# Kernel tuning notes

Measured on AMD Instinct MI355X. Metric: run time of the kernel, lower is better.

Reference implementation:

```python
import jax, jax.numpy as jnp
import numpy as np

N_EMBD = 768
HEAD_SIZE = 64

def setup_inputs() -> dict:
    key = jax.random.key(0)
    k1, k2, k3, k4 = jax.random.split(key, 4)
    B, T = 8, 2048
    x = jax.random.normal(k1, (B, T, N_EMBD), dtype=jnp.float32)
    s = 1.0 / np.sqrt(N_EMBD)
    Wk = jax.random.normal(k2, (N_EMBD, HEAD_SIZE), dtype=jnp.float32) * s
    Wq = jax.random.normal(k3, (N_EMBD, HEAD_SIZE), dtype=jnp.float32) * s
    Wv = jax.random.normal(k4, (N_EMBD, HEAD_SIZE), dtype=jnp.float32) * s
    return {"x": x, "Wk": Wk, "Wq": Wq, "Wv": Wv}

def reference(x, Wk, Wq, Wv):
    # x: [B, T, C]; projections: [B, T, H]
    B, T, C = x.shape
    k = jnp.einsum('btc,ch->bth', x, Wk)
    q = jnp.einsum('btc,ch->bth', x, Wq)
    v = jnp.einsum('btc,ch->bth', x, Wv)
    # scores [B, T, T], scaled by head_size^-0.5
    wei = jnp.einsum('bth,bsh->bts', q, k) * (HEAD_SIZE ** -0.5)
    causal = jnp.tril(jnp.ones((T, T), dtype=bool))
    wei = jnp.where(causal, wei, -jnp.inf)
    wei = jax.nn.softmax(wei, axis=-1)
    # dropout omitted (eval mode / deterministic reference)
    out = jnp.einsum('bts,bsh->bth', wei, v)
    return out
```

## Files before the change

### kernel.cpp

```cpp
#include <hip/hip_runtime.h>

#define B_ 8
#define T_ 2048
#define C_ 768
#define H_ 64
#define QT_ (T_ / 64)
#define NCH_ 8

typedef __bf16 bf16x8 __attribute__((ext_vector_type(8)));
typedef unsigned short ushort8 __attribute__((ext_vector_type(8)));
typedef float f32x4 __attribute__((ext_vector_type(4)));
typedef float f32x16 __attribute__((ext_vector_type(16)));

typedef __attribute__((address_space(1))) const void g_void;
typedef __attribute__((address_space(3))) void lds_void;

static __device__ __forceinline__ unsigned short f32_to_bf16(float f) {
  unsigned int u = __float_as_uint(f);
  u += 0x7FFFu + ((u >> 16) & 1u);
  return (unsigned short)(u >> 16);
}

static __device__ __forceinline__ float bf16_to_f32(unsigned short u) {
  return __uint_as_float(((unsigned int)u) << 16);
}

static __device__ __forceinline__ unsigned int cvtpk_bf16(float a, float b) {
  unsigned int r;
  asm("v_cvt_pk_bf16_f32 %0, %1, %2" : "=v"(r) : "v"(a), "v"(b));
  return r;
}

static __device__ __forceinline__ f32x4 mfma16(ushort8 a, ushort8 b, f32x4 c) {
  return __builtin_amdgcn_mfma_f32_16x16x32_bf16(
      __builtin_bit_cast(bf16x8, a), __builtin_bit_cast(bf16x8, b), c, 0, 0, 0);
}

static __device__ __forceinline__ f32x16 mfma32(ushort8 a, ushort8 b, f32x16 c) {
  return __builtin_amdgcn_mfma_f32_32x32x16_bf16(
      __builtin_bit_cast(bf16x8, a), __builtin_bit_cast(bf16x8, b), c, 0, 0, 0);
}

template <int BASE>
static __device__ __forceinline__ ushort8 packA(const f32x16& p) {
  unsigned int a1 = cvtpk_bf16(p[BASE + 0], p[BASE + 1]);
  unsigned int a2 = cvtpk_bf16(p[BASE + 2], p[BASE + 3]);
  unsigned int a3 = cvtpk_bf16(p[BASE + 4], p[BASE + 5]);
  unsigned int a4 = cvtpk_bf16(p[BASE + 6], p[BASE + 7]);
  asm("v_permlane32_swap_b32 %0, %1" : "+v"(a1), "+v"(a3));
  asm("v_permlane32_swap_b32 %0, %1" : "+v"(a2), "+v"(a4));
  uint4 w = {a1, a2, a3, a4};
  return __builtin_bit_cast(ushort8, w);
}

__global__ void prep_w_kernel(const float* __restrict__ Wk, const float* __restrict__ Wq,
                              const float* __restrict__ Wv, unsigned short* __restrict__ Wt) {
  int g = blockIdx.x * 256 + threadIdx.x;
  if (g >= 24 * 768) return;
  int ks = g / 768, s = g - ks * 768;
  int n = s >> 2, perm = s & 3;
  int k8 = perm ^ (n & 3) ^ ((n >> 2) & 3);
  int p = n >> 6, col = n & 63;
  const float* W = (p == 0) ? Wk : (p == 1) ? Wq : Wv;
  float sc = (p == 1) ? 0.125f * 1.44269504088896f : 1.0f;
  int kbase = ks * 32 + k8 * 8;
  ushort8 v;
#pragma unroll
  for (int e = 0; e < 8; ++e) v[e] = f32_to_bf16(W[(kbase + e) * 64 + col] * sc);
  *(ushort8*)(Wt + (size_t)g * 8) = v;
}

__global__ __launch_bounds__(512) void proj_kernel(
    const float* __restrict__ x, const unsigned short* __restrict__ Wt,
    unsigned short* __restrict__ Qb, unsigned short* __restrict__ Kb,
    unsigned short* __restrict__ Vt) {
  __shared__ unsigned short Wl[2][6144];
  __shared__ unsigned short Xl[2][1024];
  const int tid = threadIdx.x;
  const int wave = tid >> 6, lane = tid & 63;
  const int lo = lane & 15, hi = lane >> 4;
  const int rg = wave & 1, ch3 = wave >> 1;
  const int row0 = blockIdx.x * 32;

  f32x4 acc[3];
#pragma unroll
  for (int t = 0; t < 3; ++t) acc[t] = (f32x4){0.f, 0.f, 0.f, 0.f};

  const int xr = (tid & 127) >> 2;
  const int xk8 = tid & 3;
  const int xslot = xr * 4 + (xk8 ^ (xr & 3) ^ ((xr >> 2) & 3));
  const float* xsrc = x + (size_t)(row0 + xr) * C_ + xk8 * 8;

  const int arow = rg * 16 + lo;
  const int aaddr = (arow * 4 + (hi ^ (arow & 3) ^ ((arow >> 2) & 3))) * 8;

  auto wstage = [&](int buf, int ks) {
    const unsigned short* base = Wt + (size_t)ks * 6144 + lane * 8;
    for (int is = wave; is < 12; is += 8)
      __builtin_amdgcn_global_load_lds((g_void*)(base + is * 512),
          (lds_void*)(&Wl[buf][is * 512]), 16, 0, 0);
  };

  float4 xa0 = {}, xa1 = {}, xb0 = {}, xb1 = {};

  wstage(0, 0);
  if (tid < 128) {
    xa0 = *(const float4*)(xsrc);
    xa1 = *(const float4*)(xsrc + 4);
  }

  for (int ks = 0; ks < 24; ++ks) {
    const int cur = ks & 1;
    asm volatile("s_waitcnt vmcnt(0)" ::: "memory");
    __syncthreads();
    if (ks + 1 < 24) {
      wstage(cur ^ 1, ks + 1);
      if (tid < 128) {
        xb0 = *(const float4*)(xsrc + (ks + 1) * 32);
        xb1 = *(const float4*)(xsrc + (ks + 1) * 32 + 4);
      }
    }
    if (tid < 128) {
      unsigned int dd[4];
      dd[0] = cvtpk_bf16(xa0.x, xa0.y);
      dd[1] = cvtpk_bf16(xa0.z, xa0.w);
      dd[2] = cvtpk_bf16(xa1.x, xa1.y);
      dd[3] = cvtpk_bf16(xa1.z, xa1.w);
      *(uint4*)(&Xl[cur][xslot * 8]) = *(uint4*)dd;
    }
    __syncthreads();
    ushort8 af = *(const ushort8*)(&Xl[cur][aaddr]);
#pragma unroll
    for (int t = 0; t < 3; ++t) {
      const int n = ch3 * 48 + t * 16 + lo;
      const int baddr = (n * 4 + (hi ^ (n & 3) ^ ((n >> 2) & 3))) * 8;
      ushort8 bfr = *(const ushort8*)(&Wl[cur][baddr]);
      acc[t] = mfma16(af, bfr, acc[t]);
    }
    xa0 = xb0; xa1 = xb1;
  }

#pragma unroll
  for (int t = 0; t < 3; ++t) {
    const int n = ch3 * 48 + t * 16 + lo;
    const int p = n >> 6, nn = n & 63;
#pragma unroll
    for (int r = 0; r < 4; ++r) {
      const int rgl = row0 + rg * 16 + hi * 4 + r;
      unsigned short val = f32_to_bf16(acc[t][r]);
      if (p == 0) {
        Kb[rgl * H_ + nn] = val;
      } else if (p == 1) {
        Qb[rgl * H_ + nn] = val;
      } else {
        const int b = rgl >> 11;
        const int tt = rgl & (T_ - 1);
        Vt[((b * H_ + nn) << 11) + tt] = val;
      }
    }
  }
}

__global__ __launch_bounds__(128) void attn_part_kernel(
    const unsigned short* __restrict__ Qb, const unsigned short* __restrict__ Kb,
    const unsigned short* __restrict__ Vt, unsigned short* __restrict__ Opb,
    float* __restrict__ Ml) {
  const int qt = blockIdx.x;
  const int b = blockIdx.y;
  const int ch = blockIdx.z;
  const int t0 = ch * 4;
  if (t0 > qt) return;
  const int t1 = min(qt, t0 + 3);

  __shared__ __align__(16) unsigned short Kl[2][4096];
  __shared__ __align__(16) unsigned short Vl[2][4096];

  const int tid = threadIdx.x;
  const int wave = tid >> 6;
  const int lane = tid & 63;
  const int il = lane & 31;
  const int h = lane >> 5;
  const int i0w = qt * 64 + wave * 32;
  const size_t bt = (size_t)b * T_;

  const int srow = tid >> 3;
  const int sslot = (tid & 7) ^ (srow & 7);

  ushort8 qf[4];
#pragma unroll
  for (int dc = 0; dc < 4; ++dc)
    qf[dc] = *(const ushort8*)(Qb + (bt + i0w + il) * 64 + dc * 16 + h * 8);

  f32x16 o0 = {}, o1 = {};
  float m = -1e30f, lsum = 0.f;

  auto stage = [&](int buf, int jt) {
    const int j0 = jt * 64;
#pragma unroll
    for (int is = 0; is < 4; ++is) {
      const unsigned short* gK = Kb + ((bt + j0 + is * 16 + srow) << 6) + (sslot << 3);
      __builtin_amdgcn_global_load_lds((g_void*)gK,
          (lds_void*)(&Kl[buf][is * 1024 + wave * 512]), 16, 0, 0);
    }
#pragma unroll
    for (int is = 0; is < 4; ++is) {
      const unsigned short* gV = Vt + (((size_t)(b * H_ + is * 16 + srow)) << 11) + j0 + (sslot << 3);
      __builtin_amdgcn_global_load_lds((g_void*)gV,
          (lds_void*)(&Vl[buf][is * 1024 + wave * 512]), 16, 0, 0);
    }
  };

  stage(0, t0);

  for (int jt = t0; jt <= t1; ++jt) {
    const int cur = (jt - t0) & 1;
    asm volatile("s_waitcnt vmcnt(0)" ::: "memory");
    __syncthreads();
    if (jt < t1) stage(cur ^ 1, jt + 1);
    const int j0 = jt * 64;

    f32x16 s0 = {}, s1 = {};
    __builtin_amdgcn_s_setprio(1);
#pragma unroll
    for (int dc = 0; dc < 4; ++dc) {
      const int swz = ((dc * 2 + h) ^ (il & 7)) << 3;
      ushort8 k0 = *(const ushort8*)(&Kl[cur][(il << 6) + swz]);
      ushort8 k1 = *(const ushort8*)(&Kl[cur][((32 + il) << 6) + swz]);
      s0 = mfma32(k0, qf[dc], s0);
      s1 = mfma32(k1, qf[dc], s1);
    }
    __builtin_amdgcn_s_setprio(0);

    if (jt == qt) {
      const int ig = i0w + il;
#pragma unroll
      for (int r = 0; r < 16; ++r) {
        const int jl = j0 + (r & 3) + 8 * (r >> 2) + 4 * h;
        if (jl > ig) s0[r] = -1e30f;
        if (jl + 32 > ig) s1[r] = -1e30f;
      }
    }

    float mx[8];
#pragma unroll
    for (int r = 0; r < 8; ++r) mx[r] = fmaxf(fmaxf(s0[r], s0[r + 8]), fmaxf(s1[r], s1[r + 8]));
#pragma unroll
    for (int d = 4; d >= 1; d >>= 1)
#pragma unroll
      for (int r = 0; r < d; ++r) mx[r] = fmaxf(mx[r], mx[r + d]);
    float tm = fmaxf(mx[0], __shfl_xor(mx[0], 32));
    const float mnew = fmaxf(m, tm);
    const float scl = exp2f(m - mnew);
    m = mnew;
    float sa = 0.f, sb = 0.f, sc2 = 0.f, sd = 0.f;
#pragma unroll
    for (int r = 0; r < 16; r += 4) {
      s0[r] = exp2f(s0[r] - mnew);     sa += s0[r];
      s0[r + 1] = exp2f(s0[r + 1] - mnew); sb += s0[r + 1];
      s0[r + 2] = exp2f(s0[r + 2] - mnew); sc2 += s0[r + 2];
      s0[r + 3] = exp2f(s0[r + 3] - mnew); sd += s0[r + 3];
    }
#pragma unroll
    for (int r = 0; r < 16; r += 4) {
      s1[r] = exp2f(s1[r] - mnew);     sa += s1[r];
      s1[r + 1] = exp2f(s1[r + 1] - mnew); sb += s1[r + 1];
      s1[r + 2] = exp2f(s1[r + 2] - mnew); sc2 += s1[r + 2];
      s1[r + 3] = exp2f(s1[r + 3] - mnew); sd += s1[r + 3];
    }
    float ts = (sa + sb) + (sc2 + sd);
    ts += __shfl_xor(ts, 32);
    lsum = lsum * scl + ts;
    o0 *= scl;
    o1 *= scl;

    __builtin_amdgcn_s_setprio(1);
#pragma unroll
    for (int c = 0; c < 4; ++c) {
      ushort8 pa = (c == 0) ? packA<0>(s0) : (c == 1) ? packA<8>(s0)
                 : (c == 2) ? packA<0>(s1) : packA<8>(s1);
      const int swz = ((c * 2 + h) ^ (il & 7)) << 3;
      ushort8 v0 = *(const ushort8*)(&Vl[cur][(il << 6) + swz]);
      ushort8 v1 = *(const ushort8*)(&Vl[cur][((32 + il) << 6) + swz]);
      o0 = mfma32(v0, pa, o0);
      o1 = mfma32(v1, pa, o1);
    }
    __builtin_amdgcn_s_setprio(0);
  }

  const size_t pb = (size_t)(b * QT_ + qt) * NCH_ + ch;
  unsigned short* op = Opb + pb * 4096 + (size_t)(wave * 32 + il) * 64;
#pragma unroll
  for (int g = 0; g < 4; ++g) {
    unsigned int w0[2], w1[2];
    w0[0] = cvtpk_bf16(o0[4 * g + 0], o0[4 * g + 1]);
    w0[1] = cvtpk_bf16(o0[4 * g + 2], o0[4 * g + 3]);
    w1[0] = cvtpk_bf16(o1[4 * g + 0], o1[4 * g + 1]);
    w1[1] = cvtpk_bf16(o1[4 * g + 2], o1[4 * g + 3]);
    *(uint2*)(op + 8 * g + 4 * h) = *(uint2*)w0;
    *(uint2*)(op + 32 + 8 * g + 4 * h) = *(uint2*)w1;
  }
  if (h == 0) {
    float* ml = Ml + pb * 128;
    ml[wave * 32 + il] = m;
    ml[64 + wave * 32 + il] = lsum;
  }
}

__global__ __launch_bounds__(256) void attn_comb_kernel(
    const unsigned short* __restrict__ Opb, const float* __restrict__ Ml,
    float* __restrict__ out) {
  const int qt = blockIdx.x;
  const int b = blockIdx.y;
  const int nc = (qt >> 2) + 1;
  const int row = threadIdx.x >> 2;
  const int c0 = (threadIdx.x & 3) * 16;
  const size_t pbase = (size_t)(b * QT_ + qt) * NCH_;

  float m_g = -1e30f;
  for (int c = 0; c < nc; ++c) m_g = fmaxf(m_g, Ml[(pbase + c) * 128 + row]);
  float l_g = 0.f;
  for (int c = 0; c < nc; ++c)
    l_g += Ml[(pbase + c) * 128 + 64 + row] * exp2f(Ml[(pbase + c) * 128 + row] - m_g);
  const float inv = 1.0f / l_g;

  f32x4 a0 = {0,0,0,0}, a1 = {0,0,0,0}, a2 = {0,0,0,0}, a3 = {0,0,0,0};
  for (int c = 0; c < nc; ++c) {
    const float wc = exp2f(Ml[(pbase + c) * 128 + row] - m_g);
    const unsigned short* op = Opb + (pbase + c) * 4096 + row * 64 + c0;
    ushort8 u0 = *(const ushort8*)(op);
    ushort8 u1 = *(const ushort8*)(op + 8);
    a0 += (f32x4){bf16_to_f32(u0[0]), bf16_to_f32(u0[1]), bf16_to_f32(u0[2]), bf16_to_f32(u0[3])} * wc;
    a1 += (f32x4){bf16_to_f32(u0[4]), bf16_to_f32(u0[5]), bf16_to_f32(u0[6]), bf16_to_f32(u0[7])} * wc;
    a2 += (f32x4){bf16_to_f32(u1[0]), bf16_to_f32(u1[1]), bf16_to_f32(u1[2]), bf16_to_f32(u1[3])} * wc;
    a3 += (f32x4){bf16_to_f32(u1[4]), bf16_to_f32(u1[5]), bf16_to_f32(u1[6]), bf16_to_f32(u1[7])} * wc;
  }
  float* o = out + ((size_t)b * T_ + qt * 64 + row) * 64 + c0;
  *(f32x4*)(o) = a0 * inv;
  *(f32x4*)(o + 4) = a1 * inv;
  *(f32x4*)(o + 8) = a2 * inv;
  *(f32x4*)(o + 12) = a3 * inv;
}

extern "C" void kernel_launch(void* const* d_in, const int* in_sizes, int n_in,
                              void* d_out, int out_size, void* d_ws, size_t ws_size,
                              hipStream_t stream) {
  const float* x = (const float*)d_in[0];
  const float* Wk = (const float*)d_in[1];
  const float* Wq = (const float*)d_in[2];
  const float* Wv = (const float*)d_in[3];
  float* out = (float*)d_out;

  char* ws = (char*)d_ws;
  unsigned short* Qb = (unsigned short*)(ws);
  unsigned short* Kb = (unsigned short*)(ws + (2u << 20));
  unsigned short* Vt = (unsigned short*)(ws + (4u << 20));
  unsigned short* Wt = (unsigned short*)(ws + (6u << 20));
  unsigned short* Opb = (unsigned short*)(ws + (8u << 20));
  float* Ml = (float*)(ws + (24u << 20));

  prep_w_kernel<<<dim3(72), dim3(256), 0, stream>>>(Wk, Wq, Wv, Wt);
  proj_kernel<<<dim3((B_ * T_) / 32), dim3(512), 0, stream>>>(x, Wt, Qb, Kb, Vt);
  attn_part_kernel<<<dim3(QT_, B_, NCH_), dim3(128), 0, stream>>>(Qb, Kb, Vt, Opb, Ml);
  attn_comb_kernel<<<dim3(QT_, B_), dim3(256), 0, stream>>>(Opb, Ml, out);
}
```

Baseline: 65.59 us.

## Store Q/K/V in MFMA fragment order and load directly into registers

The projection kernel now writes Q, K and V in a layout that matches per-lane MFMA operand order. The attention kernel can then load each lane's 16-byte fragment straight from global memory into registers. This removes the LDS staging buffers, the double-buffer pipeline and the barriers. The cost is no explicit prefetch overlap: the global loads for each tile are issued at the top of the iteration, with no cross-tile double buffering. The projection epilogue also does scattered 2-byte stores into the new layout.

```diff
diff --git a/kernel.cpp b/kernel.cpp
--- a/kernel.cpp
+++ b/kernel.cpp
@@ -72,8 +72,8 @@
 
 __global__ __launch_bounds__(512) void proj_kernel(
     const float* __restrict__ x, const unsigned short* __restrict__ Wt,
-    unsigned short* __restrict__ Qb, unsigned short* __restrict__ Kb,
-    unsigned short* __restrict__ Vt) {
+    unsigned short* __restrict__ Qf, unsigned short* __restrict__ Kf,
+    unsigned short* __restrict__ Vf) {
   __shared__ unsigned short Wl[2][6144];
   __shared__ unsigned short Xl[2][1024];
   const int tid = threadIdx.x;
@@ -143,27 +143,29 @@
 #pragma unroll
   for (int t = 0; t < 3; ++t) {
     const int n = ch3 * 48 + t * 16 + lo;
-    const int p = n >> 6, nn = n & 63;
+    const int p = n >> 6, d = n & 63;
 #pragma unroll
     for (int r = 0; r < 4; ++r) {
       const int rgl = row0 + rg * 16 + hi * 4 + r;
+      const int b = rgl >> 11;
+      const int tt = rgl & (T_ - 1);
       unsigned short val = f32_to_bf16(acc[t][r]);
-      if (p == 0) {
-        Kb[rgl * H_ + nn] = val;
-      } else if (p == 1) {
-        Qb[rgl * H_ + nn] = val;
+      if (p == 2) {
+        const size_t addr = ((((size_t)b * 128 + (tt >> 4)) * 2 + (d >> 5)) * 64 +
+                             ((tt >> 3) & 1) * 32 + (d & 31)) * 8 + (tt & 7);
+        Vf[addr] = val;
       } else {
-        const int b = rgl >> 11;
-        const int tt = rgl & (T_ - 1);
-        Vt[((b * H_ + nn) << 11) + tt] = val;
+        const size_t addr = ((((size_t)b * 64 + (tt >> 5)) * 4 + (d >> 4)) * 64 +
+                             ((d >> 3) & 1) * 32 + (tt & 31)) * 8 + (d & 7);
+        if (p == 0) Kf[addr] = val; else Qf[addr] = val;
       }
     }
   }
 }
 
 __global__ __launch_bounds__(128) void attn_part_kernel(
-    const unsigned short* __restrict__ Qb, const unsigned short* __restrict__ Kb,
-    const unsigned short* __restrict__ Vt, unsigned short* __restrict__ Opb,
+    const unsigned short* __restrict__ Qf, const unsigned short* __restrict__ Kf,
+    const unsigned short* __restrict__ Vf, unsigned short* __restrict__ Opb,
     float* __restrict__ Ml) {
   const int qt = blockIdx.x;
   const int b = blockIdx.y;
@@ -172,62 +174,48 @@
   if (t0 > qt) return;
   const int t1 = min(qt, t0 + 3);
 
-  __shared__ __align__(16) unsigned short Kl[2][4096];
-  __shared__ __align__(16) unsigned short Vl[2][4096];
-
   const int tid = threadIdx.x;
   const int wave = tid >> 6;
   const int lane = tid & 63;
   const int il = lane & 31;
   const int h = lane >> 5;
   const int i0w = qt * 64 + wave * 32;
-  const size_t bt = (size_t)b * T_;
-
-  const int srow = tid >> 3;
-  const int sslot = (tid & 7) ^ (srow & 7);
+
+  const unsigned short* qbase = Qf + ((((size_t)b * 64 + (qt * 2 + wave)) * 4) << 9) + lane * 8;
+  const unsigned short* kbase = Kf + (((size_t)b * 64) << 11) + lane * 8;
+  const unsigned short* vbase = Vf + (((size_t)b * 128) << 10) + lane * 8;
 
   ushort8 qf[4];
 #pragma unroll
-  for (int dc = 0; dc < 4; ++dc)
-    qf[dc] = *(const ushort8*)(Qb + (bt + i0w + il) * 64 + dc * 16 + h * 8);
+  for (int dc = 0; dc < 4; ++dc) qf[dc] = *(const ushort8*)(qbase + (dc << 9));
 
   f32x16 o0 = {}, o1 = {};
   float m = -1e30f, lsum = 0.f;
 
-  auto stage = [&](int buf, int jt) {
+  for (int jt = t0; jt <= t1; ++jt) {
     const int j0 = jt * 64;
-#pragma unroll
-    for (int is = 0; is < 4; ++is) {
-      const unsigned short* gK = Kb + ((bt + j0 + is * 16 + srow) << 6) + (sslot << 3);
-      __builtin_amdgcn_global_load_lds((g_void*)gK,
-          (lds_void*)(&Kl[buf][is * 1024 + wave * 512]), 16, 0, 0);
-    }
-#pragma unroll
-    for (int is = 0; is < 4; ++is) {
-      const unsigned short* gV = Vt + (((size_t)(b * H_ + is * 16 + srow)) << 11) + j0 + (sslot << 3);
-      __builtin_amdgcn_global_load_lds((g_void*)gV,
-          (lds_void*)(&Vl[buf][is * 1024 + wave * 512]), 16, 0, 0);
-    }
-  };
-
-  stage(0, t0);
-
-  for (int jt = t0; jt <= t1; ++jt) {
-    const int cur = (jt - t0) & 1;
-    asm volatile("s_waitcnt vmcnt(0)" ::: "memory");
-    __syncthreads();
-    if (jt < t1) stage(cur ^ 1, jt + 1);
-    const int j0 = jt * 64;
+    const size_t jg = (size_t)(jt * 2);
+
+    ushort8 kf0[4], kf1[4];
+#pragma unroll
+    for (int dc = 0; dc < 4; ++dc) {
+      kf0[dc] = *(const ushort8*)(kbase + (jg << 11) + (dc << 9));
+      kf1[dc] = *(const ushort8*)(kbase + ((jg + 1) << 11) + (dc << 9));
+    }
+    ushort8 vf0[4], vf1[4];
+#pragma unroll
+    for (int c = 0; c < 4; ++c) {
+      const size_t jc = (size_t)(jt * 4 + c);
+      vf0[c] = *(const ushort8*)(vbase + (jc << 10));
+      vf1[c] = *(const ushort8*)(vbase + (jc << 10) + (1 << 9));
+    }
 
     f32x16 s0 = {}, s1 = {};
     __builtin_amdgcn_s_setprio(1);
 #pragma unroll
     for (int dc = 0; dc < 4; ++dc) {
-      const int swz = ((dc * 2 + h) ^ (il & 7)) << 3;
-      ushort8 k0 = *(const ushort8*)(&Kl[cur][(il << 6) + swz]);
-      ushort8 k1 = *(const ushort8*)(&Kl[cur][((32 + il) << 6) + swz]);
-      s0 = mfma32(k0, qf[dc], s0);
-      s1 = mfma32(k1, qf[dc], s1);
+      s0 = mfma32(kf0[dc], qf[dc], s0);
+      s1 = mfma32(kf1[dc], qf[dc], s1);
     }
     __builtin_amdgcn_s_setprio(0);
 
@@ -278,11 +266,8 @@
     for (int c = 0; c < 4; ++c) {
       ushort8 pa = (c == 0) ? packA<0>(s0) : (c == 1) ? packA<8>(s0)
                  : (c == 2) ? packA<0>(s1) : packA<8>(s1);
-      const int swz = ((c * 2 + h) ^ (il & 7)) << 3;
-      ushort8 v0 = *(const ushort8*)(&Vl[cur][(il << 6) + swz]);
-      ushort8 v1 = *(const ushort8*)(&Vl[cur][((32 + il) << 6) + swz]);
-      o0 = mfma32(v0, pa, o0);
-      o1 = mfma32(v1, pa, o1);
+      o0 = mfma32(vf0[c], pa, o0);
+      o1 = mfma32(vf1[c], pa, o1);
     }
     __builtin_amdgcn_s_setprio(0);
   }
@@ -351,15 +336,15 @@
   float* out = (float*)d_out;
 
   char* ws = (char*)d_ws;
-  unsigned short* Qb = (unsigned short*)(ws);
-  unsigned short* Kb = (unsigned short*)(ws + (2u << 20));
-  unsigned short* Vt = (unsigned short*)(ws + (4u << 20));
+  unsigned short* Qf = (unsigned short*)(ws);
+  unsigned short* Kf = (unsigned short*)(ws + (2u << 20));
+  unsigned short* Vf = (unsigned short*)(ws + (4u << 20));
   unsigned short* Wt = (unsigned short*)(ws + (6u << 20));
   unsigned short* Opb = (unsigned short*)(ws + (8u << 20));
   float* Ml = (float*)(ws + (24u << 20));
 
   prep_w_kernel<<<dim3(72), dim3(256), 0, stream>>>(Wk, Wq, Wv, Wt);
-  proj_kernel<<<dim3((B_ * T_) / 32), dim3(512), 0, stream>>>(x, Wt, Qb, Kb, Vt);
-  attn_part_kernel<<<dim3(QT_, B_, NCH_), dim3(128), 0, stream>>>(Qb, Kb, Vt, Opb, Ml);
+  proj_kernel<<<dim3((B_ * T_) / 32), dim3(512), 0, stream>>>(x, Wt, Qf, Kf, Vf);
+  attn_part_kernel<<<dim3(QT_, B_, NCH_), dim3(128), 0, stream>>>(Qf, Kf, Vf, Opb, Ml);
   attn_comb_kernel<<<dim3(QT_, B_), dim3(256), 0, stream>>>(Opb, Ml, out);
 }
```

Result: faster. 59.68 us (-9.0%).
